# Performance work log

Measured on AMD Instinct MI355X. Metric: run time of the kernel, lower is better.

## Reference

```python
import jax, jax.numpy as jnp
import numpy as np

PI = np.pi
NQ = 9  # qubits: edge 0-2, node 3-6 (center=3, neighbor0=4), anc1=7, anc2=8


def _mlp(x, W1, b1, W2, b2):
    h = jax.nn.leaky_relu(x @ W1 + b1, negative_slope=0.2)
    return h @ W2 + b2


def _ry(t):
    h = 0.5 * t
    c = jnp.cos(h).astype(jnp.complex64)
    s = jnp.sin(h).astype(jnp.complex64)
    return jnp.stack([jnp.stack([c, -s]), jnp.stack([s, c])])


def _rx(t):
    h = 0.5 * t
    c = jnp.cos(h).astype(jnp.complex64)
    s = jnp.sin(h).astype(jnp.complex64)
    return jnp.stack([jnp.stack([c, -1j * s]), jnp.stack([-1j * s, c])])


def _rz(t):
    h = (0.5 * t).astype(jnp.complex64)
    e = jnp.exp(-1j * h)
    z = jnp.zeros((), jnp.complex64)
    return jnp.stack([jnp.stack([e, z]), jnp.stack([z, jnp.conj(e)])])


def _ap1(state, U, q):
    s = jnp.moveaxis(state, q, 0)
    s = jnp.tensordot(U, s, axes=([1], [0]))
    return jnp.moveaxis(s, 0, q)


def _apc(state, U, c, t):  # controlled-U, control c, target t
    s = jnp.moveaxis(state, (c, t), (0, 1))
    s1 = jnp.tensordot(U, s[1], axes=([1], [0]))
    s = jnp.stack([s[0], s1])
    return jnp.moveaxis(s, (0, 1), (c, t))


def _cz(state, a, b):
    s = jnp.moveaxis(state, (a, b), (0, 1))
    s = s.at[1, 1].multiply(-1.0)
    return jnp.moveaxis(s, (0, 1), (a, b))


def _pqc(data, theta):
    # data: [18] per-graphlet angles, theta: [27] shared weights; returns <X_center>
    state = jnp.zeros((2,) * NQ, jnp.complex64).at[(0,) * NQ].set(1.0)
    for i in range(3):  # edge qubits: ry, rz
        state = _ap1(state, _ry(data[2 * i]), i)
        state = _ap1(state, _rz(data[2 * i + 1]), i)
    for i in range(4):  # node qubits: ry, rz
        state = _ap1(state, _ry(data[6 + 2 * i]), 3 + i)
        state = _ap1(state, _rz(data[7 + 2 * i]), 3 + i)
    state = _apc(state, _rx(data[14]), 4, 7)  # neighbor -> anc1, c-rx(phi0)
    state = _apc(state, _ry(data[15]), 0, 7)  # edge0    -> anc1, c-ry(phi1)
    state = _apc(state, _rz(data[16]), 4, 8)  # neighbor -> anc2, c-rz(phi2)
    state = _apc(state, _ry(data[17]), 0, 8)  # edge0    -> anc2, c-ry(phi3)
    for b, qs in enumerate([(0, 4, 7), (7, 4, 8), (3, 7, 8)]):  # A, B, U blocks
        th = theta[9 * b:9 * b + 9]
        for i, q in enumerate(qs):
            state = _ap1(state, _rx(th[3 * i + 0]), q)
            state = _ap1(state, _ry(th[3 * i + 1]), q)
            state = _ap1(state, _rz(th[3 * i + 2]), q)
        state = _cz(state, qs[0], qs[1])
        state = _cz(state, qs[1], qs[2])
        state = _cz(state, qs[2], qs[0])
    xs = jnp.moveaxis(jnp.moveaxis(state, 3, 0)[::-1], 0, 3)  # apply X on qubit 3
    return jnp.real(jnp.vdot(state, xs)).astype(jnp.float32)


def setup_inputs() -> dict:
    N, E, K, G = 6000, 96000, 4, 32
    rng = np.random.default_rng(0)
    src = rng.integers(0, N, E)
    dst = (src + 1 + rng.integers(0, N - 1, E)) % N  # no self loops
    pairs = np.stack([np.minimum(src, dst), np.maximum(src, dst)], 1)
    keymap = {(int(u), int(v)): i for i, (u, v) in enumerate(pairs)}
    und = np.unique(np.concatenate([np.stack([src, dst], 1), np.stack([dst, src], 1)], 0), axis=0)
    deg = np.bincount(und[:, 0], minlength=N)
    starts = np.concatenate([[0], np.cumsum(deg)])[:-1]
    gn = np.full((N, K), -1, np.int32)
    gn[:, 0] = np.arange(N)
    ge = np.full((N, K - 1), -1, np.int32)
    for j in range(K - 1):
        has = deg > j
        cs = np.nonzero(has)[0]
        nb = und[starts[has] + j, 1]
        gn[cs, 1 + j] = nb
        for c, n in zip(cs.tolist(), nb.tolist()):
            ge[c, j] = keymap[(min(c, n), max(c, n))]
    batch = ((np.arange(N) * G) // N).astype(np.int32)
    key = jax.random.key(0)
    ks = jax.random.split(key, 12)

    def dense(k, i, o):
        return jax.random.normal(k, (i, o), jnp.float32) / np.sqrt(i)

    return dict(
        node_feat=jax.random.normal(ks[0], (N, 16), jnp.float32),
        edge_attr=jax.random.normal(ks[1], (E, 8), jnp.float32),
        node_W1=dense(ks[2], 16, 128), node_b1=jnp.zeros((128,), jnp.float32),
        node_W2=dense(ks[3], 128, 2), node_b2=jnp.zeros((2,), jnp.float32),
        edge_W1=dense(ks[4], 8, 128), edge_b1=jnp.zeros((128,), jnp.float32),
        edge_W2=dense(ks[5], 128, 2), edge_b2=jnp.zeros((2,), jnp.float32),
        theta=jax.random.uniform(ks[6], (1, 27), jnp.float32, -0.1, 0.1),
        upd_W1=dense(ks[7], 3, 128)[None], upd_b1=jnp.zeros((1, 128), jnp.float32),
        upd_W2=dense(ks[8], 128, 2)[None], upd_b2=jnp.zeros((1, 2), jnp.float32),
        head_W1=dense(ks[9], 2, 2), head_b1=jnp.zeros((2,), jnp.float32),
        head_W2=dense(ks[10], 2, 2), head_b2=jnp.zeros((2,), jnp.float32),
        graphlet_nodes=jnp.asarray(gn), graphlet_edges=jnp.asarray(ge),
        batch=jnp.asarray(batch), num_graphs=G,
    )


def reference(node_feat, edge_attr, node_W1, node_b1, node_W2, node_b2,
              edge_W1, edge_b1, edge_W2, edge_b2, theta,
              upd_W1, upd_b1, upd_W2, upd_b2,
              head_W1, head_b1, head_W2, head_b2,
              graphlet_nodes, graphlet_edges, batch, num_graphs):
    node_f = jnp.tanh(_mlp(node_feat, node_W1, node_b1, node_W2, node_b2)) * PI
    edge_f = jnp.tanh(_mlp(edge_attr, edge_W1, edge_b1, edge_W2, edge_b2)) * PI
    nm = (graphlet_nodes >= 0).astype(node_f.dtype)[..., None]  # pad mask
    em = (graphlet_edges >= 0).astype(edge_f.dtype)[..., None]
    gn = jnp.clip(graphlet_nodes, 0)
    ge = jnp.clip(graphlet_edges, 0)
    N = node_f.shape[0]
    e_feat = edge_f[ge] * em  # [N,3,2] fixed across hops
    for h in range(theta.shape[0]):
        n_feat = node_f[gn] * nm  # [N,4,2]
        phis = jnp.stack([n_feat[:, 1, 0], e_feat[:, 0, 0], n_feat[:, 1, 1], e_feat[:, 0, 1]], 1)
        data = jnp.concatenate([e_feat.reshape(N, 6), n_feat.reshape(N, 8), phis], 1)  # [N,18]
        exp = jax.vmap(_pqc, in_axes=(0, None))(data, theta[h])  # [N]
        upd_inp = jnp.concatenate([node_f[gn[:, 0]], exp[:, None]], 1)  # [N,3]
        upd = _mlp(upd_inp, upd_W1[h], upd_b1[h], upd_W2[h], upd_b2[h])  # [N,2]
        node_f = node_f + jnp.zeros_like(node_f).at[gn[:, 0]].add(upd)
    seg = jax.ops.segment_sum(node_f, batch, num_segments=num_graphs)
    cnt = jax.ops.segment_sum(jnp.ones((N,), node_f.dtype), batch, num_segments=num_graphs)
    emb = seg / cnt[:, None]  # global mean pool
    return _mlp(emb, head_W1, head_b1, head_W2, head_b2)
```

## Files before the change

### kernel.cpp

```cpp
#include <hip/hip_runtime.h>

#define PI_F 3.14159265358979323846f

struct C2 { float r, i; };
struct M2 { C2 m[2][2]; };

__device__ __forceinline__ C2 cmul(C2 a, C2 b){ return C2{a.r*b.r - a.i*b.i, a.r*b.i + a.i*b.r}; }
__device__ __forceinline__ C2 cadd(C2 a, C2 b){ return C2{a.r+b.r, a.i+b.i}; }

__device__ __forceinline__ M2 mmul(M2 A, M2 B){
  M2 R;
  #pragma unroll
  for (int r=0;r<2;++r)
    #pragma unroll
    for (int c=0;c<2;++c)
      R.m[r][c] = cadd(cmul(A.m[r][0],B.m[0][c]), cmul(A.m[r][1],B.m[1][c]));
  return R;
}
__device__ __forceinline__ M2 m_rz(float t){ float s,c; __sincosf(0.5f*t,&s,&c);
  M2 U; U.m[0][0]=C2{c,-s}; U.m[0][1]=C2{0,0}; U.m[1][0]=C2{0,0}; U.m[1][1]=C2{c,s}; return U; }
__device__ __forceinline__ M2 m_ry(float t){ float s,c; __sincosf(0.5f*t,&s,&c);
  M2 U; U.m[0][0]=C2{c,0}; U.m[0][1]=C2{-s,0}; U.m[1][0]=C2{s,0}; U.m[1][1]=C2{c,0}; return U; }
__device__ __forceinline__ M2 m_rx(float t){ float s,c; __sincosf(0.5f*t,&s,&c);
  M2 U; U.m[0][0]=C2{c,0}; U.m[0][1]=C2{0,-s}; U.m[1][0]=C2{0,-s}; U.m[1][1]=C2{c,0}; return U; }
__device__ __forceinline__ M2 fuse_zyx(float tz, float ty, float tx){ return mmul(m_rz(tz), mmul(m_ry(ty), m_rx(tx))); }

__device__ __forceinline__ float fast_tanh(float x){
  float e = __expf(2.f*x);
  return 1.f - 2.f/(e + 1.f);
}

__device__ __forceinline__ M2 loadM(const float* __restrict__ p){
  M2 U;
  U.m[0][0]=C2{p[0],p[1]}; U.m[0][1]=C2{p[2],p[3]};
  U.m[1][0]=C2{p[4],p[5]}; U.m[1][1]=C2{p[6],p[7]};
  return U;
}


template<int T>
__device__ __forceinline__ void applyT16(M2 U, float (&sr)[16], float (&si)[16]){
  #pragma unroll
  for (int a0=0;a0<16;++a0){
    if (a0 & T) continue;
    const int a1 = a0 | T;
    C2 x0{sr[a0], si[a0]}, x1{sr[a1], si[a1]};
    C2 n0 = cadd(cmul(U.m[0][0],x0), cmul(U.m[0][1],x1));
    C2 n1 = cadd(cmul(U.m[1][0],x0), cmul(U.m[1][1],x1));
    sr[a0]=n0.r; si[a0]=n0.i; sr[a1]=n1.r; si[a1]=n1.i;
  }
}

__device__ __forceinline__ void applyQ0(M2 U, int p, float (&sr)[16], float (&si)[16]){
  const float u0r = p ? U.m[1][0].r : U.m[0][0].r;
  const float u0i = p ? U.m[1][0].i : U.m[0][0].i;
  const float u1r = p ? U.m[1][1].r : U.m[0][1].r;
  const float u1i = p ? U.m[1][1].i : U.m[0][1].i;
  #pragma unroll
  for (int a=0;a<16;++a){
    const float orr = __shfl_xor(sr[a], 1);
    const float oii = __shfl_xor(si[a], 1);
    const float xar = p ? orr   : sr[a], xai = p ? oii   : si[a];
    const float xbr = p ? sr[a] : orr,   xbi = p ? si[a] : oii;
    sr[a] = u0r*xar - u0i*xai + u1r*xbr - u1i*xbi;
    si[a] = u0r*xai + u0i*xar + u1r*xbi + u1i*xbr;
  }
}

template<int BA,int BB,int BC>
__device__ __forceinline__ void czTriple16(float (&sr)[16], float (&si)[16]){
  #pragma unroll
  for (int a=0;a<16;++a){
    const int x=(a&BA)?1:0, y=(a&BB)?1:0, z=(a&BC)?1:0;
    if (((x&y)^(y&z)^(z&x)) != 0){ sr[a]=-sr[a]; si[a]=-si[a]; }
  }
}

__global__ void features_kernel(const float* __restrict__ node_feat,
                                const float* __restrict__ edge_attr,
                                const int* __restrict__ ge,
                                const float* __restrict__ nW1, const float* __restrict__ nb1,
                                const float* __restrict__ nW2, const float* __restrict__ nb2,
                                const float* __restrict__ eW1, const float* __restrict__ eb1,
                                const float* __restrict__ eW2, const float* __restrict__ eb2,
                                float* __restrict__ node_f, float* __restrict__ ef,
                                int N,
                                const float* __restrict__ theta, float* __restrict__ tm){
  const int row = blockIdx.x*blockDim.x + threadIdx.x;
  if (row < 9){
    M2 U = fuse_zyx(theta[3*row+2], theta[3*row+1], theta[3*row+0]);
    float* p = tm + row*8;
    p[0]=U.m[0][0].r; p[1]=U.m[0][0].i;
    p[2]=U.m[0][1].r; p[3]=U.m[0][1].i;
    p[4]=U.m[1][0].r; p[5]=U.m[1][0].i;
    p[6]=U.m[1][1].r; p[7]=U.m[1][1].i;
  }
  if (row < N){
    const float4* nf4 = reinterpret_cast<const float4*>(node_feat + (size_t)row*16);
    const float4 A = nf4[0], B = nf4[1], C = nf4[2], D = nf4[3];
    const float xi[16] = {A.x,A.y,A.z,A.w, B.x,B.y,B.z,B.w,
                          C.x,C.y,C.z,C.w, D.x,D.y,D.z,D.w};
    float a0 = nb2[0], a1 = nb2[1];
    #pragma unroll 4
    for (int j=0;j<128;++j){
      float h = nb1[j];
      #pragma unroll
      for (int i=0;i<16;++i) h = fmaf(xi[i], nW1[i*128+j], h);
      h = h > 0.f ? h : 0.2f*h;
      a0 = fmaf(h, nW2[j*2+0], a0);
      a1 = fmaf(h, nW2[j*2+1], a1);
    }
    node_f[row*2+0] = PI_F * fast_tanh(a0);
    node_f[row*2+1] = PI_F * fast_tanh(a1);
  } else {
    const int r = row - N;
    if (r >= N) return;
    const int e = ge[r*3+0];
    if (e < 0){ ef[r*2+0] = 0.f; ef[r*2+1] = 0.f; return; }
    const float4* ea4 = reinterpret_cast<const float4*>(edge_attr + (size_t)e*8);
    const float4 A = ea4[0], B = ea4[1];
    const float xi[8] = {A.x,A.y,A.z,A.w, B.x,B.y,B.z,B.w};
    float a0 = eb2[0], a1 = eb2[1];
    #pragma unroll 4
    for (int j=0;j<128;++j){
      float h = eb1[j];
      #pragma unroll
      for (int i=0;i<8;++i) h = fmaf(xi[i], eW1[i*128+j], h);
      h = h > 0.f ? h : 0.2f*h;
      a0 = fmaf(h, eW2[j*2+0], a0);
      a1 = fmaf(h, eW2[j*2+1], a1);
    }
    ef[r*2+0] = PI_F * fast_tanh(a0);
    ef[r*2+1] = PI_F * fast_tanh(a1);
  }
}

__global__ void __launch_bounds__(64, 1)
pqc_kernel(const float* __restrict__ node_f, const float* __restrict__ ef,
           const int* __restrict__ gn,
           const float* __restrict__ tm,
           const float* __restrict__ uW1, const float* __restrict__ ub1,
           const float* __restrict__ uW2, const float* __restrict__ ub2,
           float* __restrict__ upd, int N){
  const int t = blockIdx.x*64 + threadIdx.x;
  const int n = t >> 1;
  const int p = t & 1;
  if (n >= N) return;

  const float e0 = ef[n*2+0], e1 = ef[n*2+1];
  const float f0 = node_f[n*2+0], f1 = node_f[n*2+1];
  const int v1 = gn[n*4+1];
  const bool ok = v1 >= 0; const int idx = ok ? v1 : 0;
  const float g0 = ok ? node_f[idx*2+0] : 0.f;
  const float g1 = ok ? node_f[idx*2+1] : 0.f;

  float sy0,cy0,sz0,cz0, sy3,cy3,sz3,cz3, sy4,cy4,sz4,cz4;
  __sincosf(0.5f*e0,&sy0,&cy0); __sincosf(0.5f*e1,&sz0,&cz0);
  __sincosf(0.5f*f0,&sy3,&cy3); __sincosf(0.5f*f1,&sz3,&cz3);
  __sincosf(0.5f*g0,&sy4,&cy4); __sincosf(0.5f*g1,&sz4,&cz4);

  const C2 v0[2] = { C2{cy0*cz0, -cy0*sz0}, C2{sy0*cz0, sy0*sz0} };
  const C2 v3[2] = { C2{cy3*cz3, -cy3*sz3}, C2{sy3*cz3, sy3*sz3} };
  const C2 v4[2] = { C2{cy4*cz4, -cy4*sz4}, C2{sy4*cz4, sy4*sz4} };
  const C2 v0p = p ? v0[1] : v0[0];

  float sr[16], si[16];
  #pragma unroll
  for (int a=0;a<16;++a){ sr[a]=0.f; si[a]=0.f; }
  #pragma unroll
  for (int b3=0;b3<2;++b3){
    const C2 tt = cmul(v0p, v3[b3]);
    #pragma unroll
    for (int b2=0;b2<2;++b2){
      const C2 a = cmul(tt, v4[b2]);
      const int ix = b3*8 + b2*4;
      sr[ix]=a.r; si[ix]=a.i;
    }
  }

  #pragma unroll
  for (int a0=0;a0<16;++a0){
    if ((a0 & 2) || !(a0 & 4)) continue;
    const int a1 = a0 | 2;
    const float r0=sr[a0], i0=si[a0], r1=sr[a1], i1=si[a1];
    sr[a0] = cy4*r0 + sy4*i1;  si[a0] = cy4*i0 - sy4*r1;
    sr[a1] = sy4*i0 + cy4*r1;  si[a1] = -sy4*r0 + cy4*i1;
  }
  {
    const float sA = p ? sy0 : 0.f, cA = p ? cy0 : 1.f;
    #pragma unroll
    for (int a0=0;a0<16;++a0){
      if (a0 & 2) continue;
      const int a1 = a0 | 2;
      const float r0=sr[a0], i0=si[a0], r1=sr[a1], i1=si[a1];
      sr[a0] = cA*r0 - sA*r1;  si[a0] = cA*i0 - sA*i1;
      sr[a1] = sA*r0 + cA*r1;  si[a1] = sA*i0 + cA*i1;
    }
  }
  #pragma unroll
  for (int a=0;a<16;++a){
    if (!(a & 4)) continue;
    const float r=sr[a], im=si[a];
    if (a & 1){ sr[a] = r*cz4 - im*sz4;  si[a] = im*cz4 + r*sz4; }
    else      { sr[a] = r*cz4 + im*sz4;  si[a] = im*cz4 - r*sz4; }
  }
  {
    const float sB = p ? sz0 : 0.f, cB = p ? cz0 : 1.f;
    #pragma unroll
    for (int a0=0;a0<16;++a0){
      if (a0 & 1) continue;
      const int a1 = a0 | 1;
      const float r0=sr[a0], i0=si[a0], r1=sr[a1], i1=si[a1];
      sr[a0] = cB*r0 - sB*r1;  si[a0] = cB*i0 - sB*i1;
      sr[a1] = sB*r0 + cB*r1;  si[a1] = sB*i0 + cB*i1;
    }
  }

  applyQ0(loadM(tm+0*8), p, sr, si);
  applyT16<4>(loadM(tm+1*8), sr, si);
  applyT16<2>(loadM(tm+2*8), sr, si);
  {
    const float sg = p ? -1.f : 1.f;
    #pragma unroll
    for (int a=0;a<16;++a){
      const int y=(a>>2)&1, z=(a>>1)&1;
      if (y & z)      { sr[a]=-sr[a];  si[a]=-si[a]; }
      else if (y | z) { sr[a]*=sg;     si[a]*=sg;    }
    }
  }
  applyT16<2>(loadM(tm+3*8), sr, si);
  applyT16<4>(loadM(tm+4*8), sr, si);
  applyT16<1>(loadM(tm+5*8), sr, si);
  czTriple16<2,4,1>(sr, si);
  applyT16<8>(loadM(tm+6*8), sr, si);
  applyT16<2>(loadM(tm+7*8), sr, si);
  applyT16<1>(loadM(tm+8*8), sr, si);
  czTriple16<8,2,1>(sr, si);

  float acc = 0.f;
  #pragma unroll
  for (int a=0;a<16;++a) acc += sr[a]*sr[a^8] + si[a]*si[a^8];
  acc += __shfl_xor(acc, 1);

  float o0 = 0.f, o1 = 0.f;
  #pragma unroll 4
  for (int jj=0;jj<64;++jj){
    const int j = 2*jj + p;
    float h = ub1[j];
    h = fmaf(f0,  uW1[0*128+j], h);
    h = fmaf(f1,  uW1[1*128+j], h);
    h = fmaf(acc, uW1[2*128+j], h);
    h = h > 0.f ? h : 0.2f*h;
    o0 = fmaf(h, uW2[j*2+0], o0);
    o1 = fmaf(h, uW2[j*2+1], o1);
  }
  o0 += __shfl_xor(o0, 1);
  o1 += __shfl_xor(o1, 1);
  if (!p){
    *reinterpret_cast<float2*>(upd + (size_t)n*2) =
        float2{f0 + ub2[0] + o0, f1 + ub2[1] + o1};
  }
}

__global__ void reduce_head_kernel(const float* __restrict__ upd,
                                   const float* __restrict__ hW1, const float* __restrict__ hb1,
                                   const float* __restrict__ hW2, const float* __restrict__ hb2,
                                   float* __restrict__ out, int N, int G){
  const int g = blockIdx.x;
  const int start = (g*N + G - 1)/G;
  const int end   = ((g+1)*N + G - 1)/G;
  float a0=0.f, a1=0.f;
  for (int n = start + threadIdx.x; n < end; n += 64){
    const float2 u = *reinterpret_cast<const float2*>(upd + (size_t)n*2);
    a0 += u.x;
    a1 += u.y;
  }
  #pragma unroll
  for (int m=32; m; m>>=1){ a0 += __shfl_xor(a0, m); a1 += __shfl_xor(a1, m); }
  if (threadIdx.x == 0){
    const float inv = 1.f / (float)(end - start);
    const float e0 = a0*inv, e1 = a1*inv;
    float h0 = hb1[0] + e0*hW1[0*2+0] + e1*hW1[1*2+0];
    float h1 = hb1[1] + e0*hW1[0*2+1] + e1*hW1[1*2+1];
    h0 = h0 > 0.f ? h0 : 0.2f*h0;
    h1 = h1 > 0.f ? h1 : 0.2f*h1;
    out[g*2+0] = hb2[0] + h0*hW2[0*2+0] + h1*hW2[1*2+0];
    out[g*2+1] = hb2[1] + h0*hW2[0*2+1] + h1*hW2[1*2+1];
  }
}

extern "C" void kernel_launch(void* const* d_in, const int* in_sizes, int n_in,
                              void* d_out, int out_size, void* d_ws, size_t ws_size,
                              hipStream_t stream) {
  const float* node_feat = (const float*)d_in[0];
  const float* edge_attr = (const float*)d_in[1];
  const float* nW1 = (const float*)d_in[2];
  const float* nb1 = (const float*)d_in[3];
  const float* nW2 = (const float*)d_in[4];
  const float* nb2 = (const float*)d_in[5];
  const float* eW1 = (const float*)d_in[6];
  const float* eb1 = (const float*)d_in[7];
  const float* eW2 = (const float*)d_in[8];
  const float* eb2 = (const float*)d_in[9];
  const float* theta = (const float*)d_in[10];
  const float* uW1 = (const float*)d_in[11];
  const float* ub1 = (const float*)d_in[12];
  const float* uW2 = (const float*)d_in[13];
  const float* ub2 = (const float*)d_in[14];
  const float* hW1 = (const float*)d_in[15];
  const float* hb1 = (const float*)d_in[16];
  const float* hW2 = (const float*)d_in[17];
  const float* hb2 = (const float*)d_in[18];
  const int* gn    = (const int*)d_in[19];
  const int* ge    = (const int*)d_in[20];

  const int N = in_sizes[0] / 16;
  const int G = out_size / 2;

  float* node_f = (float*)d_ws;
  float* ef     = node_f + (size_t)N*2;
  float* upd    = ef + (size_t)N*2;
  float* tm     = upd + (size_t)N*2;

  const int R = 2*N;
  features_kernel<<<(R+255)/256, 256, 0, stream>>>(node_feat, edge_attr, ge,
                                                   nW1, nb1, nW2, nb2,
                                                   eW1, eb1, eW2, eb2,
                                                   node_f, ef, N, theta, tm);
  pqc_kernel<<<(2*N+63)/64, 64, 0, stream>>>(node_f, ef, gn, tm,
                                             uW1, ub1, uW2, ub2, upd, N);
  reduce_head_kernel<<<G, 64, 0, stream>>>(upd,
                                           hW1, hb1, hW2, hb2, (float*)d_out, N, G);
}
```

Measured before the change: 133.4 us.

## Split PQC state and MLPs across four lanes per graphlet

```diff
diff --git a/kernel.cpp b/kernel.cpp
--- a/kernel.cpp
+++ b/kernel.cpp
@@ -39,9 +39,9 @@
 
 
 template<int T>
-__device__ __forceinline__ void applyT16(M2 U, float (&sr)[16], float (&si)[16]){
-  #pragma unroll
-  for (int a0=0;a0<16;++a0){
+__device__ __forceinline__ void applyT8(M2 U, float (&sr)[8], float (&si)[8]){
+  #pragma unroll
+  for (int a0=0;a0<8;++a0){
     if (a0 & T) continue;
     const int a1 = a0 | T;
     C2 x0{sr[a0], si[a0]}, x1{sr[a1], si[a1]};
@@ -51,15 +51,16 @@
   }
 }
 
-__device__ __forceinline__ void applyQ0(M2 U, int p, float (&sr)[16], float (&si)[16]){
+template<int XORMASK>
+__device__ __forceinline__ void applySplit(M2 U, int p, float (&sr)[8], float (&si)[8]){
   const float u0r = p ? U.m[1][0].r : U.m[0][0].r;
   const float u0i = p ? U.m[1][0].i : U.m[0][0].i;
   const float u1r = p ? U.m[1][1].r : U.m[0][1].r;
   const float u1i = p ? U.m[1][1].i : U.m[0][1].i;
   #pragma unroll
-  for (int a=0;a<16;++a){
-    const float orr = __shfl_xor(sr[a], 1);
-    const float oii = __shfl_xor(si[a], 1);
+  for (int a=0;a<8;++a){
+    const float orr = __shfl_xor(sr[a], XORMASK);
+    const float oii = __shfl_xor(si[a], XORMASK);
     const float xar = p ? orr   : sr[a], xai = p ? oii   : si[a];
     const float xbr = p ? sr[a] : orr,   xbi = p ? si[a] : oii;
     sr[a] = u0r*xar - u0i*xai + u1r*xbr - u1i*xbi;
@@ -68,11 +69,22 @@
 }
 
 template<int BA,int BB,int BC>
-__device__ __forceinline__ void czTriple16(float (&sr)[16], float (&si)[16]){
-  #pragma unroll
-  for (int a=0;a<16;++a){
+__device__ __forceinline__ void czTriple8(float (&sr)[8], float (&si)[8]){
+  #pragma unroll
+  for (int a=0;a<8;++a){
     const int x=(a&BA)?1:0, y=(a&BB)?1:0, z=(a&BC)?1:0;
     if (((x&y)^(y&z)^(z&x)) != 0){ sr[a]=-sr[a]; si[a]=-si[a]; }
+  }
+}
+
+template<int BY,int BZ>
+__device__ __forceinline__ void czSplit(int p, float (&sr)[8], float (&si)[8]){
+  const float sg = p ? -1.f : 1.f;
+  #pragma unroll
+  for (int a=0;a<8;++a){
+    const int y=(a&BY)?1:0, z=(a&BZ)?1:0;
+    if (y & z)      { sr[a]=-sr[a];  si[a]=-si[a]; }
+    else if (y | z) { sr[a]*=sg;     si[a]*=sg;    }
   }
 }
 
@@ -86,10 +98,12 @@
                                 float* __restrict__ node_f, float* __restrict__ ef,
                                 int N,
                                 const float* __restrict__ theta, float* __restrict__ tm){
-  const int row = blockIdx.x*blockDim.x + threadIdx.x;
-  if (row < 9){
-    M2 U = fuse_zyx(theta[3*row+2], theta[3*row+1], theta[3*row+0]);
-    float* p = tm + row*8;
+  const int t = blockIdx.x*blockDim.x + threadIdx.x;
+  const int row = t >> 2;
+  const int q   = t & 3;
+  if (t < 9){
+    M2 U = fuse_zyx(theta[3*t+2], theta[3*t+1], theta[3*t+0]);
+    float* p = tm + t*8;
     p[0]=U.m[0][0].r; p[1]=U.m[0][0].i;
     p[2]=U.m[0][1].r; p[3]=U.m[0][1].i;
     p[4]=U.m[1][0].r; p[5]=U.m[1][0].i;
@@ -100,9 +114,10 @@
     const float4 A = nf4[0], B = nf4[1], C = nf4[2], D = nf4[3];
     const float xi[16] = {A.x,A.y,A.z,A.w, B.x,B.y,B.z,B.w,
                           C.x,C.y,C.z,C.w, D.x,D.y,D.z,D.w};
-    float a0 = nb2[0], a1 = nb2[1];
+    float a0 = 0.f, a1 = 0.f;
     #pragma unroll 4
-    for (int j=0;j<128;++j){
+    for (int jj=0;jj<32;++jj){
+      const int j = 4*jj + q;
       float h = nb1[j];
       #pragma unroll
       for (int i=0;i<16;++i) h = fmaf(xi[i], nW1[i*128+j], h);
@@ -110,19 +125,24 @@
       a0 = fmaf(h, nW2[j*2+0], a0);
       a1 = fmaf(h, nW2[j*2+1], a1);
     }
-    node_f[row*2+0] = PI_F * fast_tanh(a0);
-    node_f[row*2+1] = PI_F * fast_tanh(a1);
+    a0 += __shfl_xor(a0,1); a0 += __shfl_xor(a0,2);
+    a1 += __shfl_xor(a1,1); a1 += __shfl_xor(a1,2);
+    if (q == 0){
+      *reinterpret_cast<float2*>(node_f + (size_t)row*2) =
+          float2{PI_F * fast_tanh(nb2[0] + a0), PI_F * fast_tanh(nb2[1] + a1)};
+    }
   } else {
     const int r = row - N;
     if (r >= N) return;
     const int e = ge[r*3+0];
-    if (e < 0){ ef[r*2+0] = 0.f; ef[r*2+1] = 0.f; return; }
+    if (e < 0){ if (q == 0){ ef[r*2+0] = 0.f; ef[r*2+1] = 0.f; } return; }
     const float4* ea4 = reinterpret_cast<const float4*>(edge_attr + (size_t)e*8);
     const float4 A = ea4[0], B = ea4[1];
     const float xi[8] = {A.x,A.y,A.z,A.w, B.x,B.y,B.z,B.w};
-    float a0 = eb2[0], a1 = eb2[1];
+    float a0 = 0.f, a1 = 0.f;
     #pragma unroll 4
-    for (int j=0;j<128;++j){
+    for (int jj=0;jj<32;++jj){
+      const int j = 4*jj + q;
       float h = eb1[j];
       #pragma unroll
       for (int i=0;i<8;++i) h = fmaf(xi[i], eW1[i*128+j], h);
@@ -130,8 +150,12 @@
       a0 = fmaf(h, eW2[j*2+0], a0);
       a1 = fmaf(h, eW2[j*2+1], a1);
     }
-    ef[r*2+0] = PI_F * fast_tanh(a0);
-    ef[r*2+1] = PI_F * fast_tanh(a1);
+    a0 += __shfl_xor(a0,1); a0 += __shfl_xor(a0,2);
+    a1 += __shfl_xor(a1,1); a1 += __shfl_xor(a1,2);
+    if (q == 0){
+      *reinterpret_cast<float2*>(ef + (size_t)r*2) =
+          float2{PI_F * fast_tanh(eb2[0] + a0), PI_F * fast_tanh(eb2[1] + a1)};
+    }
   }
 }
 
@@ -142,9 +166,10 @@
            const float* __restrict__ uW1, const float* __restrict__ ub1,
            const float* __restrict__ uW2, const float* __restrict__ ub2,
            float* __restrict__ upd, int N){
-  const int t = blockIdx.x*64 + threadIdx.x;
-  const int n = t >> 1;
-  const int p = t & 1;
+  const int t  = blockIdx.x*64 + threadIdx.x;
+  const int n  = t >> 2;
+  const int p0 = t & 1;
+  const int p1 = (t >> 1) & 1;
   if (n >= N) return;
 
   const float e0 = ef[n*2+0], e1 = ef[n*2+1];
@@ -162,24 +187,19 @@
   const C2 v0[2] = { C2{cy0*cz0, -cy0*sz0}, C2{sy0*cz0, sy0*sz0} };
   const C2 v3[2] = { C2{cy3*cz3, -cy3*sz3}, C2{sy3*cz3, sy3*sz3} };
   const C2 v4[2] = { C2{cy4*cz4, -cy4*sz4}, C2{sy4*cz4, sy4*sz4} };
-  const C2 v0p = p ? v0[1] : v0[0];
-
-  float sr[16], si[16];
-  #pragma unroll
-  for (int a=0;a<16;++a){ sr[a]=0.f; si[a]=0.f; }
-  #pragma unroll
-  for (int b3=0;b3<2;++b3){
-    const C2 tt = cmul(v0p, v3[b3]);
-    #pragma unroll
-    for (int b2=0;b2<2;++b2){
-      const C2 a = cmul(tt, v4[b2]);
-      const int ix = b3*8 + b2*4;
-      sr[ix]=a.r; si[ix]=a.i;
-    }
-  }
-
-  #pragma unroll
-  for (int a0=0;a0<16;++a0){
+  const C2 vv = cmul(p0 ? v0[1] : v0[0], p1 ? v3[1] : v3[0]);
+
+  float sr[8], si[8];
+  #pragma unroll
+  for (int a=0;a<8;++a){ sr[a]=0.f; si[a]=0.f; }
+  #pragma unroll
+  for (int b2=0;b2<2;++b2){
+    const C2 a = cmul(vv, v4[b2]);
+    sr[b2*4]=a.r; si[b2*4]=a.i;
+  }
+
+  #pragma unroll
+  for (int a0=0;a0<8;++a0){
     if ((a0 & 2) || !(a0 & 4)) continue;
     const int a1 = a0 | 2;
     const float r0=sr[a0], i0=si[a0], r1=sr[a1], i1=si[a1];
@@ -187,9 +207,9 @@
     sr[a1] = sy4*i0 + cy4*r1;  si[a1] = -sy4*r0 + cy4*i1;
   }
   {
-    const float sA = p ? sy0 : 0.f, cA = p ? cy0 : 1.f;
+    const float sA = p0 ? sy0 : 0.f, cA = p0 ? cy0 : 1.f;
     #pragma unroll
-    for (int a0=0;a0<16;++a0){
+    for (int a0=0;a0<8;++a0){
       if (a0 & 2) continue;
       const int a1 = a0 | 2;
       const float r0=sr[a0], i0=si[a0], r1=sr[a1], i1=si[a1];
@@ -198,16 +218,16 @@
     }
   }
   #pragma unroll
-  for (int a=0;a<16;++a){
+  for (int a=0;a<8;++a){
     if (!(a & 4)) continue;
     const float r=sr[a], im=si[a];
     if (a & 1){ sr[a] = r*cz4 - im*sz4;  si[a] = im*cz4 + r*sz4; }
     else      { sr[a] = r*cz4 + im*sz4;  si[a] = im*cz4 - r*sz4; }
   }
   {
-    const float sB = p ? sz0 : 0.f, cB = p ? cz0 : 1.f;
+    const float sB = p0 ? sz0 : 0.f, cB = p0 ? cz0 : 1.f;
     #pragma unroll
-    for (int a0=0;a0<16;++a0){
+    for (int a0=0;a0<8;++a0){
       if (a0 & 1) continue;
       const int a1 = a0 | 1;
       const float r0=sr[a0], i0=si[a0], r1=sr[a1], i1=si[a1];
@@ -216,36 +236,34 @@
     }
   }
 
-  applyQ0(loadM(tm+0*8), p, sr, si);
-  applyT16<4>(loadM(tm+1*8), sr, si);
-  applyT16<2>(loadM(tm+2*8), sr, si);
-  {
-    const float sg = p ? -1.f : 1.f;
-    #pragma unroll
-    for (int a=0;a<16;++a){
-      const int y=(a>>2)&1, z=(a>>1)&1;
-      if (y & z)      { sr[a]=-sr[a];  si[a]=-si[a]; }
-      else if (y | z) { sr[a]*=sg;     si[a]*=sg;    }
-    }
-  }
-  applyT16<2>(loadM(tm+3*8), sr, si);
-  applyT16<4>(loadM(tm+4*8), sr, si);
-  applyT16<1>(loadM(tm+5*8), sr, si);
-  czTriple16<2,4,1>(sr, si);
-  applyT16<8>(loadM(tm+6*8), sr, si);
-  applyT16<2>(loadM(tm+7*8), sr, si);
-  applyT16<1>(loadM(tm+8*8), sr, si);
-  czTriple16<8,2,1>(sr, si);
+  applySplit<1>(loadM(tm+0*8), p0, sr, si);
+  applyT8<4>(loadM(tm+1*8), sr, si);
+  applyT8<2>(loadM(tm+2*8), sr, si);
+  czSplit<4,2>(p0, sr, si);
+  applyT8<2>(loadM(tm+3*8), sr, si);
+  applyT8<4>(loadM(tm+4*8), sr, si);
+  applyT8<1>(loadM(tm+5*8), sr, si);
+  czTriple8<2,4,1>(sr, si);
+  applySplit<2>(loadM(tm+6*8), p1, sr, si);
+  applyT8<2>(loadM(tm+7*8), sr, si);
+  applyT8<1>(loadM(tm+8*8), sr, si);
+  czSplit<2,1>(p1, sr, si);
 
   float acc = 0.f;
   #pragma unroll
-  for (int a=0;a<16;++a) acc += sr[a]*sr[a^8] + si[a]*si[a^8];
+  for (int a=0;a<8;++a){
+    const float pr = __shfl_xor(sr[a], 2);
+    const float pi = __shfl_xor(si[a], 2);
+    acc += sr[a]*pr + si[a]*pi;
+  }
   acc += __shfl_xor(acc, 1);
-
+  acc += __shfl_xor(acc, 2);
+
+  const int q = t & 3;
   float o0 = 0.f, o1 = 0.f;
   #pragma unroll 4
-  for (int jj=0;jj<64;++jj){
-    const int j = 2*jj + p;
+  for (int jj=0;jj<32;++jj){
+    const int j = 4*jj + q;
     float h = ub1[j];
     h = fmaf(f0,  uW1[0*128+j], h);
     h = fmaf(f1,  uW1[1*128+j], h);
@@ -254,9 +272,9 @@
     o0 = fmaf(h, uW2[j*2+0], o0);
     o1 = fmaf(h, uW2[j*2+1], o1);
   }
-  o0 += __shfl_xor(o0, 1);
-  o1 += __shfl_xor(o1, 1);
-  if (!p){
+  o0 += __shfl_xor(o0, 1); o0 += __shfl_xor(o0, 2);
+  o1 += __shfl_xor(o1, 1); o1 += __shfl_xor(o1, 2);
+  if (q == 0){
     *reinterpret_cast<float2*>(upd + (size_t)n*2) =
         float2{f0 + ub2[0] + o0, f1 + ub2[1] + o1};
   }
@@ -322,12 +340,12 @@
   float* upd    = ef + (size_t)N*2;
   float* tm     = upd + (size_t)N*2;
 
-  const int R = 2*N;
-  features_kernel<<<(R+255)/256, 256, 0, stream>>>(node_feat, edge_attr, ge,
-                                                   nW1, nb1, nW2, nb2,
-                                                   eW1, eb1, eW2, eb2,
-                                                   node_f, ef, N, theta, tm);
-  pqc_kernel<<<(2*N+63)/64, 64, 0, stream>>>(node_f, ef, gn, tm,
+  const int FT = 4*(2*N);
+  features_kernel<<<(FT+255)/256, 256, 0, stream>>>(node_feat, edge_attr, ge,
+                                                    nW1, nb1, nW2, nb2,
+                                                    eW1, eb1, eW2, eb2,
+                                                    node_f, ef, N, theta, tm);
+  pqc_kernel<<<(4*N+63)/64, 64, 0, stream>>>(node_f, ef, gn, tm,
                                              uW1, ub1, uW2, ub2, upd, N);
   reduce_head_kernel<<<G, 64, 0, stream>>>(upd,
                                            hW1, hb1, hW2, hb2, (float*)d_out, N, G);
```

Result: faster. 115.0 us (-13.8%).
